# Optimization experiments

Hardware: AMD Instinct MI355X
Metric: run time of the kernel (lower is better)

## Reference

```python
import jax, jax.numpy as jnp
import numpy as np

TEMP = 0.5  # temperature_f from init


def setup_inputs() -> dict:
    key = jax.random.key(0)
    k1, k2, k3 = jax.random.split(key, 3)
    B, d = 4096, 128
    h_i = jax.random.normal(k1, (B, d), dtype=jnp.float32)
    h_j = jax.random.normal(k2, (B, d), dtype=jnp.float32)
    S = jax.random.uniform(k3, (B, B), dtype=jnp.float32)
    return {"h_i": h_i, "h_j": h_j, "S": S}


def reference(h_i, h_j, S):
    B = h_i.shape[0]
    N = 2 * B
    h = jnp.concatenate([h_i, h_j], axis=0)                 # [N, d]
    sim = jnp.matmul(h, h.T) / TEMP                          # [N, N]
    # S_2 = 1 - (S**2).repeat(2,2); sim1 = sim * S_2
    S2 = 1.0 - jnp.tile(S * S, (2, 2))                       # [N, N]
    sim1 = sim * S2
    # positives: diag(sim, +B) and diag(sim, -B)
    idx = jnp.arange(B)
    pos = jnp.concatenate([sim[idx, idx + B], sim[idx + B, idx]])  # [N]
    # negatives mask: exclude diagonal and the positive-pair positions
    i = jnp.arange(N)[:, None]
    j = jnp.arange(N)[None, :]
    neg_mask = ~((i == j) | (j == (i + B) % N))              # [N, N], N-2 True per row
    neg = jnp.where(neg_mask, sim1, -jnp.inf)                # masked entries drop out of logsumexp
    # CrossEntropy(label=0, reduction='sum') over logits=[pos, negatives]:
    # loss_n = logsumexp(logits_n) - pos_n  (order of negatives is irrelevant)
    logits = jnp.concatenate([pos[:, None], neg], axis=1)    # [N, N-1] effective
    lse = jax.nn.logsumexp(logits, axis=1)
    loss = jnp.sum(lse - pos) / N
    return loss
```

## Files before the change

kernel.cpp:

```cpp
#include <hip/hip_runtime.h>
#include <hip/hip_bf16.h>

#define B_ROWS 4096
#define NN     8192
#define DD     128
#define NSPLIT 32
#define TSTEPS 4
#define CSHIFT 128.0f

typedef __attribute__((ext_vector_type(8))) short s8v;
typedef __attribute__((ext_vector_type(4))) float f4v;
typedef __attribute__((ext_vector_type(2))) float f2v;
typedef __attribute__((ext_vector_type(4))) unsigned short u16x4;
typedef unsigned int u32;

static constexpr float SCALE_H = 1.6986436f;
static constexpr float SCALE2  = 2.8853900818f;
static constexpr float LN2     = 0.6931471805599453f;

__device__ __forceinline__ float fast_exp2(float x) {
#if __has_builtin(__builtin_amdgcn_exp2f)
    return __builtin_amdgcn_exp2f(x);
#else
    return exp2f(x);
#endif
}

__device__ __forceinline__ unsigned short s2m_pack(float x, bool msk) {
    float s2 = msk ? 0.f : 1.f - x * x;
    union { __hip_bfloat16 h; unsigned short u; } cv;
    cv.h = __float2bfloat16(s2);
    return cv.u;
}

typedef __attribute__((address_space(1))) const u32 gu32;
typedef __attribute__((address_space(3))) u32 lu32;
__device__ __forceinline__ void gload_lds16(const void* g, void* l) {
    __builtin_amdgcn_global_load_lds((gu32*)g, (lu32*)l, 16, 0, 0);
}

__global__ void hpos_kernel(const float* __restrict__ hi, const float* __restrict__ hj,
                            __hip_bfloat16* __restrict__ hb, float* __restrict__ pos2) {
    int w = threadIdx.x >> 6, l = threadIdx.x & 63;
    int row = blockIdx.x * 4 + w;
    f2v a = ((const f2v*)(hi + (size_t)row * DD))[l];
    f2v b = ((const f2v*)(hj + (size_t)row * DD))[l];
    float d = a[0] * b[0] + a[1] * b[1];
    #pragma unroll
    for (int off = 32; off; off >>= 1) d += __shfl_xor(d, off, 64);
    if (l == 0) pos2[row] = SCALE2 * d;
    union { ushort2 u2; __hip_bfloat16 h[2]; } ua, ub;
    ua.h[0] = __float2bfloat16(a[0] * SCALE_H);
    ua.h[1] = __float2bfloat16(a[1] * SCALE_H);
    ub.h[0] = __float2bfloat16(b[0] * SCALE_H);
    ub.h[1] = __float2bfloat16(b[1] * SCALE_H);
    ((ushort2*)(hb + (size_t)row * DD))[l] = ua.u2;
    ((ushort2*)(hb + (size_t)(row + B_ROWS) * DD))[l] = ub.u2;
}

__global__ __launch_bounds__(512, 4)
void main_kernel(const __hip_bfloat16* __restrict__ hb, const float* __restrict__ S,
                 float* __restrict__ ssplit) {
    __shared__ short ldsB[2][64][128];
    __shared__ unsigned short sPn[64][128];

    const int tid = threadIdx.x;
    const int l  = tid & 63;
    const int w  = tid >> 6;
    const int wm = w >> 1, wn = w & 1;
    const int rb = blockIdx.x & 63;
    const int cs = blockIdx.x >> 6;
    const int r0 = rb * 64 + wm * 16;
    const int c0 = cs * 128;
    const int lc = l & 15;
    const int lk = l >> 4;

    const s8v* hb8 = (const s8v*)hb;

#define STAGE(BUF, T) do {                                                        \
    _Pragma("unroll")                                                             \
    for (int i = 0; i < 2; i++) {                                                 \
        const int seg  = w * 2 + i;                                    \
        const int lrw  = seg * 4 + lk;                       \
        const int grow = c0 + (T) * 32 + ((lrw < 32) ? lrw : (lrw - 32 + B_ROWS));\
        const int sc16 = lc ^ (lrw & 7);                  \
        gload_lds16((const char*)hb + ((size_t)grow << 8) + (sc16 << 4),          \
                    (char*)&ldsB[BUF][seg * 4][0]);                               \
    }                                                                             \
} while (0)

    STAGE(0, 0);

    f4v sv[4];
    const int lr = tid >> 5;
    const int cb = (tid & 31) * 4;
    {
        const float* gS = S + (size_t)(rb * 64 + lr) * B_ROWS + c0 + cb;
        #pragma unroll
        for (int k = 0; k < 4; k++)
            sv[k] = *(const f4v*)(gS + (size_t)(k * 16) * B_ROWS);
    }

    s8v afr[2][4];
    #pragma unroll
    for (int fm = 0; fm < 2; fm++) {
        int ar = r0 + lc + fm * B_ROWS;
        #pragma unroll
        for (int kk = 0; kk < 4; kk++)
            afr[fm][kk] = hb8[ar * 16 + kk * 4 + lk];
    }

    {
        const int grw0 = rb * 64 + lr;
        const int gcb  = c0 + cb;
        #pragma unroll
        for (int k = 0; k < 4; k++) {
            u16x4 p;
            #pragma unroll
            for (int e = 0; e < 4; e++)
                p[e] = s2m_pack(sv[k][e], gcb + e == grw0 + k * 16);
            *(u16x4*)&sPn[lr + k * 16][cb] = p;
        }
    }
    __syncthreads();

    float ssum[2][4];
    #pragma unroll
    for (int fm = 0; fm < 2; fm++)
        #pragma unroll
        for (int r = 0; r < 4; r++) ssum[fm][r] = 0.f;

    const char* bp[4];
    {
        const char* bb = (const char*)ldsB + (wn * 16 + lc) * 256;
        #pragma unroll
        for (int kk = 0; kk < 4; kk++)
            bp[kk] = bb + (((kk * 4 + lk) ^ (lc & 7)) << 4);
    }

#define COMPUTE(BUF, T) do {                                                      \
    f4v acc[2][2];                                                                \
    _Pragma("unroll")                                                             \
    for (int fm = 0; fm < 2; fm++)                                                \
        _Pragma("unroll")                                                         \
        for (int fh = 0; fh < 2; fh++) acc[fm][fh] = f4v{0.f, 0.f, 0.f, 0.f};     \
    _Pragma("unroll")                                                             \
    for (int kk = 0; kk < 4; kk++) {                                              \
        s8v bf0 = *(const s8v*)(bp[kk] + ((BUF) * 16384));                        \
        s8v bf1 = *(const s8v*)(bp[kk] + ((BUF) * 16384 + 8192));                 \
        _Pragma("unroll")                                                         \
        for (int fm = 0; fm < 2; fm++) {                                          \
            acc[fm][0] = __builtin_amdgcn_mfma_f32_16x16x32_bf16(                 \
                afr[fm][kk], bf0, acc[fm][0], 0, 0, 0);                           \
            acc[fm][1] = __builtin_amdgcn_mfma_f32_16x16x32_bf16(                 \
                afr[fm][kk], bf1, acc[fm][1], 0, 0, 0);                           \
        }                                                                         \
    }                                                                             \
    const int pcol = (T) * 32 + wn * 16 + lc;                                     \
    _Pragma("unroll")                                                             \
    for (int r = 0; r < 4; r++) {                                                 \
        const int prow = wm * 16 + lk * 4 + r;                                    \
        const float s2 = __uint_as_float(((u32)sPn[prow][pcol]) << 16);           \
        _Pragma("unroll")                                                         \
        for (int fm = 0; fm < 2; fm++) {                                          \
            float e0 = fast_exp2(fmaf(acc[fm][0][r], s2, -CSHIFT));               \
            float e1 = fast_exp2(fmaf(acc[fm][1][r], s2, -CSHIFT));               \
            ssum[fm][r] += e0 + e1;                                               \
        }                                                                         \
    }                                                                             \
} while (0)

    STAGE(1, 1); COMPUTE(0, 0); __syncthreads();
    STAGE(0, 2); COMPUTE(1, 1); __syncthreads();
    STAGE(1, 3); COMPUTE(0, 2); __syncthreads();
                 COMPUTE(1, 3);

#undef STAGE
#undef COMPUTE

    float* sexb = (float*)&ldsB[0][0][0];
    #pragma unroll
    for (int fm = 0; fm < 2; fm++) {
        #pragma unroll
        for (int r = 0; r < 4; r++) {
            float ss = ssum[fm][r];
            #pragma unroll
            for (int off = 1; off < 16; off <<= 1)
                ss += __shfl_xor(ss, off, 64);
            if (lc == 0) {
                int rho = wm * 16 + lk * 4 + r;
                sexb[wn * 128 + fm * 64 + rho] = ss;
            }
        }
    }
    __syncthreads();
    if (tid < 128) {
        int fm = tid >> 6, rho = tid & 63;
        float ss = sexb[fm * 64 + rho] + sexb[128 + fm * 64 + rho];
        int gr = rb * 64 + rho + fm * B_ROWS;
        ssplit[cs * NN + gr] = ss;
    }
}

__global__ __launch_bounds__(256)
void reduce_kernel(const float* __restrict__ ssplit, const float* __restrict__ pos2,
                   float* __restrict__ partial) {
    __shared__ float red[256];
    const int n = blockIdx.x * 256 + threadIdx.x;
    float p = pos2[n & (B_ROWS - 1)];
    float Ssum = fast_exp2(p - CSHIFT);
    #pragma unroll
    for (int sp = 0; sp < NSPLIT; sp++)
        Ssum += ssplit[sp * NN + n];
    red[threadIdx.x] = (CSHIFT + log2f(Ssum)) - p;
    __syncthreads();
    for (int st = 128; st; st >>= 1) {
        if (threadIdx.x < st) red[threadIdx.x] += red[threadIdx.x + st];
        __syncthreads();
    }
    if (threadIdx.x == 0) partial[blockIdx.x] = red[0];
}

__global__ void final_kernel(const float* __restrict__ partial, float* __restrict__ out) {
    if (threadIdx.x == 0) {
        float s = 0.f;
        #pragma unroll
        for (int i = 0; i < 32; i++) s += partial[i];
        out[0] = s * (LN2 / (float)NN);
    }
}

extern "C" void kernel_launch(void* const* d_in, const int* in_sizes, int n_in,
                              void* d_out, int out_size, void* d_ws, size_t ws_size,
                              hipStream_t stream) {
    (void)in_sizes; (void)n_in; (void)out_size; (void)ws_size;
    const float* hi = (const float*)d_in[0];
    const float* hj = (const float*)d_in[1];
    const float* S  = (const float*)d_in[2];

    char* ws = (char*)d_ws;
    __hip_bfloat16* hb = (__hip_bfloat16*)ws;
    float* pos2   = (float*)(ws + 2097152);
    float* ssplit = (float*)(ws + 2097152 + 16384);
    float* partial= (float*)(ws + 2097152 + 16384 + 1048576);

    hpos_kernel<<<1024, 256, 0, stream>>>(hi, hj, hb, pos2);
    main_kernel<<<2048, 512, 0, stream>>>(hb, S, ssplit);
    reduce_kernel<<<32, 256, 0, stream>>>(ssplit, pos2, partial);
    final_kernel<<<1, 64, 0, stream>>>(partial, (float*)d_out);
}
```

Before: 52.62 us.

## Exploit Gram matrix symmetry: compute upper-triangle tiles, accumulate row and column sums

```diff
diff --git a/kernel.cpp b/kernel.cpp
--- a/kernel.cpp
+++ b/kernel.cpp
@@ -4,8 +4,8 @@
 #define B_ROWS 4096
 #define NN     8192
 #define DD     128
-#define NSPLIT 32
-#define TSTEPS 4
+#define NSPLIT 64
+#define SPA    68
 #define CSHIFT 128.0f
 
 typedef __attribute__((ext_vector_type(8))) short s8v;
@@ -31,6 +31,10 @@
     union { __hip_bfloat16 h; unsigned short u; } cv;
     cv.h = __float2bfloat16(s2);
     return cv.u;
+}
+
+__device__ __forceinline__ float bf16f(unsigned short u) {
+    return __uint_as_float(((u32)u) << 16);
 }
 
 typedef __attribute__((address_space(1))) const u32 gu32;
@@ -61,144 +65,152 @@
 __global__ __launch_bounds__(512, 4)
 void main_kernel(const __hip_bfloat16* __restrict__ hb, const float* __restrict__ S,
                  float* __restrict__ ssplit) {
-    __shared__ short ldsB[2][64][128];
-    __shared__ unsigned short sPn[64][128];
+    __shared__ short ldsB[128][128];
+    __shared__ unsigned short sA[64][SPA];
+    __shared__ unsigned short sB[64][SPA];
+    __shared__ float mrg[768];
+
+    const int bid = blockIdx.x;
+    const int i = bid >> 6, j = bid & 63;
+    if (i > j) return;
+    const bool diag = (i == j);
 
     const int tid = threadIdx.x;
     const int l  = tid & 63;
     const int w  = tid >> 6;
     const int wm = w >> 1, wn = w & 1;
-    const int rb = blockIdx.x & 63;
-    const int cs = blockIdx.x >> 6;
-    const int r0 = rb * 64 + wm * 16;
-    const int c0 = cs * 128;
     const int lc = l & 15;
     const int lk = l >> 4;
+    const int r64 = i * 64, c64 = j * 64;
 
     const s8v* hb8 = (const s8v*)hb;
 
-#define STAGE(BUF, T) do {                                                        \
-    _Pragma("unroll")                                                             \
-    for (int i = 0; i < 2; i++) {                                                 \
-        const int seg  = w * 2 + i;                                    \
-        const int lrw  = seg * 4 + lk;                       \
-        const int grow = c0 + (T) * 32 + ((lrw < 32) ? lrw : (lrw - 32 + B_ROWS));\
-        const int sc16 = lc ^ (lrw & 7);                  \
-        gload_lds16((const char*)hb + ((size_t)grow << 8) + (sc16 << 4),          \
-                    (char*)&ldsB[BUF][seg * 4][0]);                               \
-    }                                                                             \
-} while (0)
-
-    STAGE(0, 0);
-
-    f4v sv[4];
-    const int lr = tid >> 5;
-    const int cb = (tid & 31) * 4;
+    #pragma unroll
+    for (int i2 = 0; i2 < 4; i2++) {
+        const int rowb = w * 16 + i2 * 4;
+        const int lrw  = rowb + lk;
+        const int grow = c64 + ((lrw < 64) ? lrw : (lrw - 64 + B_ROWS));
+        const int sc16 = lc ^ (lrw & 7);
+        gload_lds16((const char*)hb + ((size_t)grow << 8) + (sc16 << 4),
+                    (char*)&ldsB[rowb][0]);
+    }
+
     {
-        const float* gS = S + (size_t)(rb * 64 + lr) * B_ROWS + c0 + cb;
-        #pragma unroll
-        for (int k = 0; k < 4; k++)
-            sv[k] = *(const f4v*)(gS + (size_t)(k * 16) * B_ROWS);
+        const int rr = tid >> 3;
+        const int c8 = (tid & 7) * 8;
+        const float* gA = S + (size_t)(r64 + rr) * B_ROWS + c64 + c8;
+        const float* gB = S + (size_t)(c64 + rr) * B_ROWS + r64 + c8;
+        f4v a0 = ((const f4v*)gA)[0], a1 = ((const f4v*)gA)[1];
+        f4v b0 = ((const f4v*)gB)[0], b1 = ((const f4v*)gB)[1];
+        u16x4 pa0, pa1, pb0, pb1;
+        #pragma unroll
+        for (int e = 0; e < 4; e++) {
+            pa0[e] = s2m_pack(a0[e], diag && (c8 + e     == rr));
+            pa1[e] = s2m_pack(a1[e], diag && (c8 + 4 + e == rr));
+            pb0[e] = s2m_pack(b0[e], false);
+            pb1[e] = s2m_pack(b1[e], false);
+        }
+        *(u16x4*)&sA[rr][c8]     = pa0;
+        *(u16x4*)&sA[rr][c8 + 4] = pa1;
+        *(u16x4*)&sB[rr][c8]     = pb0;
+        *(u16x4*)&sB[rr][c8 + 4] = pb1;
     }
 
     s8v afr[2][4];
     #pragma unroll
     for (int fm = 0; fm < 2; fm++) {
-        int ar = r0 + lc + fm * B_ROWS;
+        int ar = (r64 + wm * 16 + lc) + fm * B_ROWS;
         #pragma unroll
         for (int kk = 0; kk < 4; kk++)
             afr[fm][kk] = hb8[ar * 16 + kk * 4 + lk];
     }
-
-    {
-        const int grw0 = rb * 64 + lr;
-        const int gcb  = c0 + cb;
-        #pragma unroll
-        for (int k = 0; k < 4; k++) {
-            u16x4 p;
-            #pragma unroll
-            for (int e = 0; e < 4; e++)
-                p[e] = s2m_pack(sv[k][e], gcb + e == grw0 + k * 16);
-            *(u16x4*)&sPn[lr + k * 16][cb] = p;
-        }
-    }
     __syncthreads();
-
-    float ssum[2][4];
-    #pragma unroll
-    for (int fm = 0; fm < 2; fm++)
-        #pragma unroll
-        for (int r = 0; r < 4; r++) ssum[fm][r] = 0.f;
 
     const char* bp[4];
     {
-        const char* bb = (const char*)ldsB + (wn * 16 + lc) * 256;
+        const char* bb = (const char*)ldsB + (wn * 32 + lc) * 256;
         #pragma unroll
         for (int kk = 0; kk < 4; kk++)
             bp[kk] = bb + (((kk * 4 + lk) ^ (lc & 7)) << 4);
     }
-
-#define COMPUTE(BUF, T) do {                                                      \
-    f4v acc[2][2];                                                                \
-    _Pragma("unroll")                                                             \
-    for (int fm = 0; fm < 2; fm++)                                                \
-        _Pragma("unroll")                                                         \
-        for (int fh = 0; fh < 2; fh++) acc[fm][fh] = f4v{0.f, 0.f, 0.f, 0.f};     \
-    _Pragma("unroll")                                                             \
-    for (int kk = 0; kk < 4; kk++) {                                              \
-        s8v bf0 = *(const s8v*)(bp[kk] + ((BUF) * 16384));                        \
-        s8v bf1 = *(const s8v*)(bp[kk] + ((BUF) * 16384 + 8192));                 \
-        _Pragma("unroll")                                                         \
-        for (int fm = 0; fm < 2; fm++) {                                          \
-            acc[fm][0] = __builtin_amdgcn_mfma_f32_16x16x32_bf16(                 \
-                afr[fm][kk], bf0, acc[fm][0], 0, 0, 0);                           \
-            acc[fm][1] = __builtin_amdgcn_mfma_f32_16x16x32_bf16(                 \
-                afr[fm][kk], bf1, acc[fm][1], 0, 0, 0);                           \
-        }                                                                         \
-    }                                                                             \
-    const int pcol = (T) * 32 + wn * 16 + lc;                                     \
-    _Pragma("unroll")                                                             \
-    for (int r = 0; r < 4; r++) {                                                 \
-        const int prow = wm * 16 + lk * 4 + r;                                    \
-        const float s2 = __uint_as_float(((u32)sPn[prow][pcol]) << 16);           \
-        _Pragma("unroll")                                                         \
-        for (int fm = 0; fm < 2; fm++) {                                          \
-            float e0 = fast_exp2(fmaf(acc[fm][0][r], s2, -CSHIFT));               \
-            float e1 = fast_exp2(fmaf(acc[fm][1][r], s2, -CSHIFT));               \
-            ssum[fm][r] += e0 + e1;                                               \
-        }                                                                         \
-    }                                                                             \
-} while (0)
-
-    STAGE(1, 1); COMPUTE(0, 0); __syncthreads();
-    STAGE(0, 2); COMPUTE(1, 1); __syncthreads();
-    STAGE(1, 3); COMPUTE(0, 2); __syncthreads();
-                 COMPUTE(1, 3);
-
-#undef STAGE
-#undef COMPUTE
-
-    float* sexb = (float*)&ldsB[0][0][0];
+    f4v acc[2][2][2];
+    #pragma unroll
+    for (int fm = 0; fm < 2; fm++)
+        #pragma unroll
+        for (int fh = 0; fh < 2; fh++)
+            #pragma unroll
+            for (int cg = 0; cg < 2; cg++) acc[fm][fh][cg] = f4v{0.f, 0.f, 0.f, 0.f};
+    #pragma unroll
+    for (int kk = 0; kk < 4; kk++) {
+        #pragma unroll
+        for (int fh = 0; fh < 2; fh++)
+            #pragma unroll
+            for (int cg = 0; cg < 2; cg++) {
+                s8v bf = *(const s8v*)(bp[kk] + fh * 16384 + cg * 4096);
+                acc[0][fh][cg] = __builtin_amdgcn_mfma_f32_16x16x32_bf16(
+                    afr[0][kk], bf, acc[0][fh][cg], 0, 0, 0);
+                acc[1][fh][cg] = __builtin_amdgcn_mfma_f32_16x16x32_bf16(
+                    afr[1][kk], bf, acc[1][fh][cg], 0, 0, 0);
+            }
+    }
+
+    float rsum[2][4], csum[2][2];
+    #pragma unroll
+    for (int fm = 0; fm < 2; fm++)
+        #pragma unroll
+        for (int r = 0; r < 4; r++) rsum[fm][r] = 0.f;
+    csum[0][0] = csum[0][1] = csum[1][0] = csum[1][1] = 0.f;
+
+    #pragma unroll
+    for (int r = 0; r < 4; r++) {
+        const int rr = wm * 16 + lk * 4 + r;
+        #pragma unroll
+        for (int cg = 0; cg < 2; cg++) {
+            const int cc = wn * 32 + cg * 16 + lc;
+            const float s2a = bf16f(sA[rr][cc]);
+            const float s2b = bf16f(sB[cc][rr]);
+            #pragma unroll
+            for (int fm = 0; fm < 2; fm++)
+                #pragma unroll
+                for (int fh = 0; fh < 2; fh++) {
+                    const float a = acc[fm][fh][cg][r];
+                    rsum[fm][r]  += fast_exp2(fmaf(a, s2a, -CSHIFT));
+                    csum[fh][cg] += fast_exp2(fmaf(a, s2b, -CSHIFT));
+                }
+        }
+    }
+
     #pragma unroll
     for (int fm = 0; fm < 2; fm++) {
         #pragma unroll
         for (int r = 0; r < 4; r++) {
-            float ss = ssum[fm][r];
-            #pragma unroll
-            for (int off = 1; off < 16; off <<= 1)
-                ss += __shfl_xor(ss, off, 64);
-            if (lc == 0) {
-                int rho = wm * 16 + lk * 4 + r;
-                sexb[wn * 128 + fm * 64 + rho] = ss;
-            }
+            float ss = rsum[fm][r];
+            #pragma unroll
+            for (int off = 1; off < 16; off <<= 1) ss += __shfl_xor(ss, off, 64);
+            if (lc == 0) mrg[wn * 128 + fm * 64 + (wm * 16 + lk * 4 + r)] = ss;
+        }
+    }
+    #pragma unroll
+    for (int fh = 0; fh < 2; fh++) {
+        #pragma unroll
+        for (int cg = 0; cg < 2; cg++) {
+            float ss = csum[fh][cg];
+            ss += __shfl_xor(ss, 16, 64);
+            ss += __shfl_xor(ss, 32, 64);
+            if (l < 16) mrg[256 + wm * 128 + fh * 64 + (wn * 32 + cg * 16 + lc)] = ss;
         }
     }
     __syncthreads();
+
     if (tid < 128) {
         int fm = tid >> 6, rho = tid & 63;
-        float ss = sexb[fm * 64 + rho] + sexb[128 + fm * 64 + rho];
-        int gr = rb * 64 + rho + fm * B_ROWS;
-        ssplit[cs * NN + gr] = ss;
+        float v = mrg[fm * 64 + rho] + mrg[128 + fm * 64 + rho];
+        ssplit[(size_t)j * NN + (r64 + rho + fm * B_ROWS)] = v;
+    } else if (!diag && tid < 256) {
+        int t2 = tid - 128, fh = t2 >> 6, cc = t2 & 63;
+        float v = mrg[256 +   0 + fh * 64 + cc] + mrg[256 + 128 + fh * 64 + cc]
+                + mrg[256 + 256 + fh * 64 + cc] + mrg[256 + 384 + fh * 64 + cc];
+        ssplit[(size_t)i * NN + (c64 + cc + fh * B_ROWS)] = v;
     }
 }
 
@@ -209,9 +221,9 @@
     const int n = blockIdx.x * 256 + threadIdx.x;
     float p = pos2[n & (B_ROWS - 1)];
     float Ssum = fast_exp2(p - CSHIFT);
-    #pragma unroll
+    #pragma unroll 8
     for (int sp = 0; sp < NSPLIT; sp++)
-        Ssum += ssplit[sp * NN + n];
+        Ssum += ssplit[(size_t)sp * NN + n];
     red[threadIdx.x] = (CSHIFT + log2f(Ssum)) - p;
     __syncthreads();
     for (int st = 128; st; st >>= 1) {
@@ -242,10 +254,10 @@
     __hip_bfloat16* hb = (__hip_bfloat16*)ws;
     float* pos2   = (float*)(ws + 2097152);
     float* ssplit = (float*)(ws + 2097152 + 16384);
-    float* partial= (float*)(ws + 2097152 + 16384 + 1048576);
+    float* partial= (float*)(ws + 2097152 + 16384 + 2097152);
 
     hpos_kernel<<<1024, 256, 0, stream>>>(hi, hj, hb, pos2);
-    main_kernel<<<2048, 512, 0, stream>>>(hb, S, ssplit);
+    main_kernel<<<4096, 512, 0, stream>>>(hb, S, ssplit);
     reduce_kernel<<<32, 256, 0, stream>>>(ssplit, pos2, partial);
     final_kernel<<<1, 64, 0, stream>>>(partial, (float*)d_out);
 }
```

After: 52.62 us. No clear change (-0.0%).
